# Kernel optimization log

Measured on AMD Instinct MI355X. Metric: run time of the kernel, lower is better.

## Reference

```python
import jax, jax.numpy as jnp
import numpy as np

H = 4096        # hidden_size
NH = 32         # heads
HD = H // NH    # head_dim = 128
EPS = 1e-5
MINUS_INF = -10000.0
B, S = 2, 1024


def setup_inputs() -> dict:
    key = jax.random.key(0)
    ks = jax.random.split(key, 7)
    x = jax.random.normal(ks[0], (B, S, H), jnp.float32)
    mask = jnp.zeros((B, 1, 1, S), jnp.float32)  # additive padding mask (0 = keep)
    norm_w = 1.0 + 0.02 * jax.random.normal(ks[1], (H,), jnp.float32)
    norm_b = 0.02 * jax.random.normal(ks[2], (H,), jnp.float32)
    qkv_w = 0.02 * jax.random.normal(ks[3], (H, 3 * H), jnp.float32)
    qkv_b = 0.02 * jax.random.normal(ks[4], (3 * H,), jnp.float32)
    attn_ow = 0.02 * jax.random.normal(ks[5], (H, H), jnp.float32)
    return {"x": x, "mask": mask, "norm_w": norm_w, "norm_b": norm_b,
            "qkv_w": qkv_w, "qkv_b": qkv_b, "attn_ow": attn_ow}


def reference(x, mask, norm_w, norm_b, qkv_w, qkv_b, attn_ow):
    b, s, h = x.shape
    # --- pre-attention layernorm (qkv_gemm fuses this in DeepSpeed) ---
    mu = jnp.mean(x, axis=-1, keepdims=True)
    var = jnp.mean(jnp.square(x - mu), axis=-1, keepdims=True)
    inp_norm = (x - mu) * jax.lax.rsqrt(var + EPS) * norm_w + norm_b
    # --- fused QKV GEMM + bias ---
    qkv = inp_norm @ qkv_w + qkv_b                      # [b, s, 3H]
    q, k, v = jnp.split(qkv, 3, axis=-1)
    q = q.reshape(b, s, NH, HD).transpose(0, 2, 1, 3)   # [b, nh, s, hd]
    k = k.reshape(b, s, NH, HD).transpose(0, 2, 1, 3)
    v = v.reshape(b, s, NH, HD).transpose(0, 2, 1, 3)
    # --- scaled dot-product with triangular (causal) mask + additive input mask ---
    norm_factor = 1.0 / jnp.sqrt(jnp.asarray(HD, x.dtype))
    scores = jnp.einsum('bhqd,bhkd->bhqk', q, k) * norm_factor  # [b, nh, s, s]
    causal = jnp.where(jnp.tril(jnp.ones((s, s), bool)), 0.0, MINUS_INF).astype(x.dtype)
    probs = jax.nn.softmax(scores + causal + mask, axis=-1)
    ctx = jnp.einsum('bhqk,bhkd->bhqd', probs, v)               # [b, nh, s, hd]
    ctx = ctx.transpose(0, 2, 1, 3).reshape(b, s, h)
    # --- output projection (vector_matmul, bias applied later in MLP residual-add) ---
    out = ctx @ attn_ow
    return out
```

## Files before the change

kernel.cpp:

```cpp
#include <hip/hip_runtime.h>
#include <stdint.h>


#define S_LEN 1024
#define HID   4096
#define NHEAD 32
#define HDIM  128

typedef __attribute__((ext_vector_type(8))) short bf16x8;
typedef __attribute__((ext_vector_type(4))) float f32x4;
typedef __attribute__((ext_vector_type(8))) unsigned short us8;

__device__ __forceinline__ unsigned short f2bf(float f) {
    union { float f; unsigned u; } v; v.f = f;
    unsigned r = v.u + 0x7fffu + ((v.u >> 16) & 1u);
    return (unsigned short)(r >> 16);
}

__device__ __forceinline__ void gld16(const unsigned short* g, unsigned short* l) {
    __builtin_amdgcn_global_load_lds(
        (const __attribute__((address_space(1))) void*)g,
        (__attribute__((address_space(3))) void*)l, 16, 0, 0);
}

__global__ __launch_bounds__(256) void ln_kernel(const float* __restrict__ x,
        const float* __restrict__ w, const float* __restrict__ bch,
        unsigned short* __restrict__ out) {
    const int row = blockIdx.x;
    const int t = threadIdx.x;
    const float* xr = x + (size_t)row * HID;
    float4 v[4];
    float sum = 0.f, sq = 0.f;
#pragma unroll
    for (int i = 0; i < 4; i++) {
        v[i] = ((const float4*)xr)[t + (i << 8)];
        sum += v[i].x + v[i].y + v[i].z + v[i].w;
        sq  += v[i].x*v[i].x + v[i].y*v[i].y + v[i].z*v[i].z + v[i].w*v[i].w;
    }
#pragma unroll
    for (int off = 32; off; off >>= 1) {
        sum += __shfl_down(sum, off);
        sq  += __shfl_down(sq, off);
    }
    __shared__ float ssum[4], ssq[4];
    if ((t & 63) == 0) { ssum[t >> 6] = sum; ssq[t >> 6] = sq; }
    __syncthreads();
    const float s_all = ssum[0] + ssum[1] + ssum[2] + ssum[3];
    const float q_all = ssq[0] + ssq[1] + ssq[2] + ssq[3];
    const float mean = s_all * (1.f / HID);
    const float var  = q_all * (1.f / HID) - mean * mean;
    const float rstd = rsqrtf(var + 1e-5f);
    unsigned short* orow = out + (size_t)row * HID;
#pragma unroll
    for (int i = 0; i < 4; i++) {
        float4 wv = ((const float4*)w)[t + (i << 8)];
        float4 bv = ((const float4*)bch)[t + (i << 8)];
        ushort4 o;
        o.x = f2bf((v[i].x - mean) * rstd * wv.x + bv.x);
        o.y = f2bf((v[i].y - mean) * rstd * wv.y + bv.y);
        o.z = f2bf((v[i].z - mean) * rstd * wv.z + bv.z);
        o.w = f2bf((v[i].w - mean) * rstd * wv.w + bv.w);
        ((ushort4*)orow)[t + (i << 8)] = o;
    }
}

__global__ __launch_bounds__(256) void transconv(const float* __restrict__ W,
        unsigned short* __restrict__ Wt, int K, int N) {
    __shared__ float tileT[128 * 65];
    const int n0 = blockIdx.x << 7, k0 = blockIdx.y << 6;
    const int t = threadIdx.x;
#pragma unroll
    for (int it = 0; it < 8; it++) {
        int idx = (it << 8) + t;
        int r = idx >> 5;
        int c4 = idx & 31;
        float4 v = *(const float4*)(W + (size_t)(k0 + r) * N + n0 + (c4 << 2));
        tileT[((c4 << 2) + 0) * 65 + r] = v.x;
        tileT[((c4 << 2) + 1) * 65 + r] = v.y;
        tileT[((c4 << 2) + 2) * 65 + r] = v.z;
        tileT[((c4 << 2) + 3) * 65 + r] = v.w;
    }
    __syncthreads();
#pragma unroll
    for (int it = 0; it < 4; it++) {
        int idx = (it << 8) + t;
        int n = idx >> 3;
        int k8 = idx & 7;
        const float* src = &tileT[n * 65 + (k8 << 3)];
        us8 o;
#pragma unroll
        for (int e = 0; e < 8; e++) o[e] = f2bf(src[e]);
        *(us8*)(Wt + (size_t)(n0 + n) * K + k0 + (k8 << 3)) = o;
    }
}


#define GEMM_PHASE(CB, KS, PFT, PFB, DO_VM)                                       \
  {                                                                               \
    bf16x8 af[4], bfv[4];                                                         \
    _Pragma("unroll") for (int ii = 0; ii < 4; ii++) af[ii] = ldA(CB, KS, ii);    \
    _Pragma("unroll") for (int jj = 0; jj < 4; jj++) bfv[jj] = ldB(CB, KS, jj);   \
    stageA(PFT, KS, PFB);                                                         \
    stageB(PFT, KS, PFB);                                                         \
    __builtin_amdgcn_s_barrier();                                                 \
    asm volatile("s_waitcnt lgkmcnt(0)" ::: "memory");                            \
    __builtin_amdgcn_sched_barrier(0);                                            \
    __builtin_amdgcn_s_setprio(1);                                                \
    _Pragma("unroll") for (int ii = 0; ii < 4; ii++)                              \
      _Pragma("unroll") for (int jj = 0; jj < 4; jj++)                            \
        acc[ii][jj] = __builtin_amdgcn_mfma_f32_16x16x32_bf16(                    \
            af[ii], bfv[jj], acc[ii][jj], 0, 0, 0);                               \
    __builtin_amdgcn_s_setprio(0);                                                \
    if (DO_VM) asm volatile("s_waitcnt vmcnt(6)" ::: "memory");                   \
    __builtin_amdgcn_s_barrier();                                                 \
  }

#define GEMM_TILE(TT, CB)                                                         \
  {                                                                               \
    int pf_ = (TT) + 2; if (pf_ > 63) pf_ = 63;                                   \
    GEMM_PHASE(CB, 0, pf_, ((CB) + 2) % 3, 0)                                     \
    GEMM_PHASE(CB, 1, pf_, ((CB) + 2) % 3, 1)                                     \
  }

__device__ __forceinline__ void gemm_core_8w(
        const unsigned short* __restrict__ GA,
        const unsigned short* __restrict__ GB,
        unsigned short* lds,
        f32x4 acc[4][4]) {
    const int t = threadIdx.x;
    const int wave = t >> 6, lane = t & 63, quad = lane >> 4, l16 = lane & 15;
    const int waveM = wave >> 2, waveN = wave & 3;
    const int srow = lane >> 2;
    const int scol = (((lane & 3) ^ ((lane >> 3) & 3)) << 3);

    auto stageA = [&](int tau, int ks, int buf) {
        const int row = (wave << 4) + srow;
        gld16(GA + ((size_t)row << 12) + (tau << 6) + (ks << 5) + scol,
              lds + buf * 24576 + (ks << 12) + (wave << 9));
    };
    auto stageB = [&](int tau, int ks, int buf) {
#pragma unroll
        for (int u = 0; u < 2; u++) {
            const int ii = (wave << 1) + u;
            const int row = (ii << 4) + srow;
            gld16(GB + ((size_t)row << 12) + (tau << 6) + (ks << 5) + scol,
                  lds + buf * 24576 + 8192 + (ks << 13) + (ii << 9));
        }
    };
    auto ldA = [&](int buf, int ks, int ii) -> bf16x8 {
        const int r = (waveM << 6) + (ii << 4) + l16;
        return ((const bf16x8*)(lds + buf * 24576 + (ks << 12)))
            [(r << 2) + (quad ^ ((r >> 1) & 3))];
    };
    auto ldB = [&](int buf, int ks, int jj) -> bf16x8 {
        const int r = (waveN << 6) + (jj << 4) + l16;
        return ((const bf16x8*)(lds + buf * 24576 + 8192 + (ks << 13)))
            [(r << 2) + (quad ^ ((r >> 1) & 3))];
    };

    stageA(0, 0, 0); stageB(0, 0, 0); stageA(0, 1, 0); stageB(0, 1, 0);
    stageA(1, 0, 1); stageB(1, 0, 1); stageA(1, 1, 1); stageB(1, 1, 1);
    asm volatile("s_waitcnt vmcnt(6)" ::: "memory");
    __builtin_amdgcn_s_barrier();

    for (int tb = 0; tb < 63; tb += 3) {
        GEMM_TILE(tb,     0)
        GEMM_TILE(tb + 1, 1)
        GEMM_TILE(tb + 2, 2)
    }
    GEMM_TILE(63, 0)
    asm volatile("s_waitcnt vmcnt(0)" ::: "memory");
}

__global__ __launch_bounds__(512, 2) void gemm_qkv8(
        const unsigned short* __restrict__ A,
        const unsigned short* __restrict__ Bt,
        const float* __restrict__ bias,
        unsigned short* __restrict__ qb,
        unsigned short* __restrict__ kb,
        unsigned short* __restrict__ vt) {
    __shared__ unsigned short lds[73728];
    const int orig = blockIdx.x;
    const int wg = ((orig & 7) * 96) + (orig >> 3);
    const int bm = wg / 48, bn = wg - bm * 48;
    const int t = threadIdx.x;
    const int wave = t >> 6, lane = t & 63, quad = lane >> 4, l16 = lane & 15;
    const int waveM = wave >> 2, waveN = wave & 3;

    const f32x4 fz = {0.f, 0.f, 0.f, 0.f};
    f32x4 acc[4][4];
#pragma unroll
    for (int i = 0; i < 4; i++)
#pragma unroll
        for (int j = 0; j < 4; j++) acc[i][j] = fz;

    gemm_core_8w(A + ((size_t)bm << 19), Bt + ((size_t)bn << 20), lds, acc);

    const int nbase = (bn << 8) + (waveN << 6);
    const int which = nbase >> 12;
#pragma unroll
    for (int ii = 0; ii < 4; ii++) {
#pragma unroll
        for (int jj = 0; jj < 4; jj++) {
#pragma unroll
            for (int r = 0; r < 4; r++) {
                int m = (bm << 7) + (waveM << 6) + (ii << 4) + (quad << 2) + r;
                int n = nbase + (jj << 4) + l16;
                float v = acc[ii][jj][r] + bias[n];
                unsigned short bvv = f2bf(v);
                int bb = m >> 10, s = m & 1023;
                int h = n & 4095, head = h >> 7, hd = h & 127;
                size_t bh = (size_t)(bb << 5) + head;
                if (which == 0)      qb[(bh * S_LEN + s) * HDIM + hd] = bvv;
                else if (which == 1) kb[(bh * S_LEN + s) * HDIM + hd] = bvv;
                else                 vt[(bh * HDIM + hd) * S_LEN + s] = bvv;
            }
        }
    }
}

__global__ __launch_bounds__(512, 2) void gemm_proj8(
        const unsigned short* __restrict__ A,
        const unsigned short* __restrict__ Bt,
        float* __restrict__ outf) {
    __shared__ unsigned short lds[73728];
    const int orig = blockIdx.x;
    const int wg = ((orig & 7) * 32) + (orig >> 3);
    const int bm = wg >> 4, bn = wg & 15;
    const int t = threadIdx.x;
    const int wave = t >> 6, lane = t & 63, quad = lane >> 4, l16 = lane & 15;
    const int waveM = wave >> 2, waveN = wave & 3;

    const f32x4 fz = {0.f, 0.f, 0.f, 0.f};
    f32x4 acc[4][4];
#pragma unroll
    for (int i = 0; i < 4; i++)
#pragma unroll
        for (int j = 0; j < 4; j++) acc[i][j] = fz;

    gemm_core_8w(A + ((size_t)bm << 19), Bt + ((size_t)bn << 20), lds, acc);

#pragma unroll
    for (int ii = 0; ii < 4; ii++)
#pragma unroll
        for (int jj = 0; jj < 4; jj++)
#pragma unroll
            for (int r = 0; r < 4; r++) {
                int m = (bm << 7) + (waveM << 6) + (ii << 4) + (quad << 2) + r;
                int n = (bn << 8) + (waveN << 6) + (jj << 4) + l16;
                outf[((size_t)m << 12) + n] = acc[ii][jj][r];
            }
}

__global__ __launch_bounds__(256) void attn_kernel(
        const unsigned short* __restrict__ qbuf,
        const unsigned short* __restrict__ kbuf,
        const unsigned short* __restrict__ vtbuf,
        const float* __restrict__ mask,
        unsigned short* __restrict__ ctx) {
    __shared__ unsigned short q_lds[64 * 128];
    __shared__ unsigned short k_lds[64 * 128];
    __shared__ unsigned short v_lds[128 * 64];
    __shared__ unsigned short p_lds[64 * 64];
    const int t = threadIdx.x;
    const int wave = t >> 6, lane = t & 63, quad = lane >> 4, l16 = lane & 15;
    const int bq = blockIdx.x, bh = blockIdx.y;
    const int q0 = bq << 6;
    const int b = bh >> 5;
    const unsigned short* Q  = qbuf  + (size_t)bh * S_LEN * HDIM;
    const unsigned short* Kp = kbuf  + (size_t)bh * S_LEN * HDIM;
    const unsigned short* Vp = vtbuf + (size_t)bh * HDIM * S_LEN;

    {
        int r = t >> 4, c = (t & 15) << 3;
#pragma unroll
        for (int it = 0; it < 4; it++)
            gld16(Q + (size_t)(q0 + r + (it << 4)) * HDIM + c,
                  q_lds + ((((it << 8) + (wave << 6))) << 3));
    }

    const f32x4 fz = {0.f, 0.f, 0.f, 0.f};
    f32x4 o[8];
#pragma unroll
    for (int n = 0; n < 8; n++) o[n] = fz;
    float l_i[4] = {0.f, 0.f, 0.f, 0.f};
    const float scale = 0.08838834764831845f;
    const float* mrow = mask + b * S_LEN;

    for (int kt = 0; kt <= bq; kt++) {
        const int k0 = kt << 6;
        {
            int rk = t >> 4, ck = (t & 15) << 3;
            int rv = t >> 3, cv = (t & 7) << 3;
#pragma unroll
            for (int it = 0; it < 4; it++) {
                gld16(Kp + (size_t)(k0 + rk + (it << 4)) * HDIM + ck,
                      k_lds + (((it << 8) + (wave << 6)) << 3));
                gld16(Vp + (size_t)(rv + (it << 5)) * S_LEN + k0 + cv,
                      v_lds + (((it << 8) + (wave << 6)) << 3));
            }
        }
        __syncthreads();

        f32x4 sacc[4];
#pragma unroll
        for (int j = 0; j < 4; j++) sacc[j] = fz;
        const bf16x8* qv = (const bf16x8*)q_lds;
        const bf16x8* kv = (const bf16x8*)k_lds;
#pragma unroll
        for (int kk = 0; kk < 4; kk++) {
            bf16x8 aq = qv[(((wave << 4) + l16) << 4) + (kk << 2) + quad];
#pragma unroll
            for (int j = 0; j < 4; j++) {
                bf16x8 bk = kv[((((j << 4) + l16)) << 4) + (kk << 2) + quad];
                sacc[j] = __builtin_amdgcn_mfma_f32_16x16x32_bf16(aq, bk, sacc[j], 0, 0, 0);
            }
        }

#pragma unroll
        for (int r = 0; r < 4; r++) {
            int qrow = q0 + (wave << 4) + (quad << 2) + r;
#pragma unroll
            for (int j = 0; j < 4; j++) {
                int key = k0 + (j << 4) + l16;
                float x = sacc[j][r] * scale + mrow[key];
                if (key > qrow) x -= 10000.0f;
                float p = __expf(x);
                l_i[r] += p;
                p_lds[((wave << 4) + (quad << 2) + r) * 64 + (j << 4) + l16] = f2bf(p);
            }
        }
        __syncthreads();

        const bf16x8* pvv = (const bf16x8*)p_lds;
        const bf16x8* vv = (const bf16x8*)v_lds;
#pragma unroll
        for (int ks = 0; ks < 2; ks++) {
            bf16x8 ap = pvv[(((wave << 4) + l16) << 3) + (ks << 2) + quad];
#pragma unroll
            for (int n = 0; n < 8; n++) {
                bf16x8 bvv = vv[((((n << 4) + l16)) << 3) + (ks << 2) + quad];
                o[n] = __builtin_amdgcn_mfma_f32_16x16x32_bf16(ap, bvv, o[n], 0, 0, 0);
            }
        }
        __syncthreads();
    }

#pragma unroll
    for (int r = 0; r < 4; r++) {
        float l = l_i[r];
#pragma unroll
        for (int off = 1; off < 16; off <<= 1) l += __shfl_xor(l, off);
        float inv = 1.0f / l;
        int qrow = q0 + (wave << 4) + (quad << 2) + r;
        size_t base = ((size_t)(b * S_LEN + qrow)) * HID + ((size_t)(bh & 31) << 7);
#pragma unroll
        for (int n = 0; n < 8; n++)
            ctx[base + (n << 4) + l16] = f2bf(o[n][r] * inv);
    }
}

extern "C" void kernel_launch(void* const* d_in, const int* in_sizes, int n_in,
                              void* d_out, int out_size, void* d_ws, size_t ws_size,
                              hipStream_t stream) {
    const float* x       = (const float*)d_in[0];
    const float* mask    = (const float*)d_in[1];
    const float* norm_w  = (const float*)d_in[2];
    const float* norm_b  = (const float*)d_in[3];
    const float* qkv_w   = (const float*)d_in[4];
    const float* qkv_b   = (const float*)d_in[5];
    const float* attn_ow = (const float*)d_in[6];
    float* out = (float*)d_out;

    char* ws = (char*)d_ws;
    size_t off = 0;
    auto alloc = [&](size_t bytes) {
        char* p = ws + off;
        off += (bytes + 255) & ~(size_t)255;
        return p;
    };
    unsigned short* inp_norm = (unsigned short*)alloc((size_t)2048 * HID * 2);
    unsigned short* qkv_wt   = (unsigned short*)alloc((size_t)3 * HID * HID * 2);
    unsigned short* ow_t     = (unsigned short*)alloc((size_t)HID * HID * 2);
    unsigned short* qb       = (unsigned short*)alloc((size_t)64 * S_LEN * HDIM * 2);
    unsigned short* kb       = (unsigned short*)alloc((size_t)64 * S_LEN * HDIM * 2);
    unsigned short* vt       = (unsigned short*)alloc((size_t)64 * S_LEN * HDIM * 2);
    unsigned short* ctx      = (unsigned short*)alloc((size_t)2048 * HID * 2);

    ln_kernel<<<2048, 256, 0, stream>>>(x, norm_w, norm_b, inp_norm);
    transconv<<<dim3(3 * HID / 128, HID / 64), 256, 0, stream>>>(qkv_w, qkv_wt, HID, 3 * HID);
    transconv<<<dim3(HID / 128, HID / 64), 256, 0, stream>>>(attn_ow, ow_t, HID, HID);
    gemm_qkv8<<<768, 512, 0, stream>>>(inp_norm, qkv_wt, qkv_b, qb, kb, vt);
    attn_kernel<<<dim3(16, 64), 256, 0, stream>>>(qb, kb, vt, mask, ctx);
    gemm_proj8<<<256, 512, 0, stream>>>(ctx, ow_t, out);
}
```

Before: 839.0 us.

## Enlarge QKV GEMM tile to 256x256 with new double-buffered core

Replaces the 128x256-tile QKV GEMM with a 256x256-tile version using a new double-buffered mainloop, where each wave computes 8x4 MFMA fragments and reuses its B fragments across two A halves. The grid drops from 768 to 384 workgroups, which halves redundant B-matrix loads and raises arithmetic intensity per LDS byte. In exchange it doubles the accumulator registers per wave, which may limit occupancy or cause spills, and 384 blocks may fill the CUs less evenly. Block ordering also changes to a simple bm-fastest mapping.

```diff
diff --git a/kernel.cpp b/kernel.cpp
--- a/kernel.cpp
+++ b/kernel.cpp
@@ -91,6 +91,127 @@
 #pragma unroll
         for (int e = 0; e < 8; e++) o[e] = f2bf(src[e]);
         *(us8*)(Wt + (size_t)(n0 + n) * K + k0 + (k8 << 3)) = o;
+    }
+}
+
+
+#define T256_PHASE(CB, KS, IH, READ_B, STAGE_CALL, DO_VM)                         \
+  {                                                                               \
+    _Pragma("unroll") for (int ii = 0; ii < 4; ii++)                              \
+        af[ii] = ldA(CB, KS, ((IH) << 2) + ii);                                   \
+    if (READ_B) {                                                                 \
+      _Pragma("unroll") for (int jj = 0; jj < 4; jj++) bfv[jj] = ldB(CB, KS, jj); \
+    }                                                                             \
+    STAGE_CALL;                                                                   \
+    __builtin_amdgcn_s_barrier();                                                 \
+    asm volatile("s_waitcnt lgkmcnt(0)" ::: "memory");                            \
+    __builtin_amdgcn_sched_barrier(0);                                            \
+    __builtin_amdgcn_s_setprio(1);                                                \
+    _Pragma("unroll") for (int ii = 0; ii < 4; ii++)                              \
+      _Pragma("unroll") for (int jj = 0; jj < 4; jj++)                            \
+        acc[((IH) << 2) + ii][jj] = __builtin_amdgcn_mfma_f32_16x16x32_bf16(      \
+            af[ii], bfv[jj], acc[((IH) << 2) + ii][jj], 0, 0, 0);                 \
+    __builtin_amdgcn_s_setprio(0);                                                \
+    if (DO_VM) asm volatile("s_waitcnt vmcnt(4)" ::: "memory");                   \
+    __builtin_amdgcn_s_barrier();                                                 \
+  }
+
+#define T256_TILE(TT, CB, PT)                                                     \
+  {                                                                               \
+    bf16x8 af[4], bfv[4];                                                         \
+    T256_PHASE(CB, 0, 0, 1, stage(GA, (((CB)^1) << 15)        , (PT), 0), 0)      \
+    T256_PHASE(CB, 0, 1, 0, stage(GB, (((CB)^1) << 15) + 16384, (PT), 0), 1)      \
+    T256_PHASE(CB, 1, 0, 1, stage(GA, (((CB)^1) << 15) +  8192, (PT), 1), 0)      \
+    T256_PHASE(CB, 1, 1, 0, stage(GB, (((CB)^1) << 15) + 24576, (PT), 1), 1)      \
+  }
+
+__device__ __forceinline__ void gemm_core_256(
+        const unsigned short* __restrict__ GA,
+        const unsigned short* __restrict__ GB,
+        unsigned short* lds,
+        f32x4 acc[8][4]) {
+    const int t = threadIdx.x;
+    const int wave = t >> 6, lane = t & 63, quad = lane >> 4, l16 = lane & 15;
+    const int waveM = wave >> 2, waveN = wave & 3;
+    const int sq8 = (((lane & 3) ^ ((lane >> 3) & 3)) << 3);
+
+    auto stage = [&](const unsigned short* G, int ldsOff, int tau, int ks) {
+#pragma unroll
+        for (int u = 0; u < 2; u++) {
+            const int grp = (u << 3) + wave;
+            const int r = (grp << 4) + (lane >> 2);
+            gld16(G + ((size_t)r << 12) + (tau << 6) + (ks << 5) + sq8,
+                  lds + ldsOff + (grp << 9));
+        }
+    };
+    auto ldA = [&](int buf, int ks, int i) -> bf16x8 {
+        const int r = (waveM << 7) + (i << 4) + l16;
+        return ((const bf16x8*)(lds + (buf << 15) + (ks << 13)))
+            [(r << 2) + (quad ^ ((r >> 1) & 3))];
+    };
+    auto ldB = [&](int buf, int ks, int j) -> bf16x8 {
+        const int r = (waveN << 6) + (j << 4) + l16;
+        return ((const bf16x8*)(lds + (buf << 15) + 16384 + (ks << 13)))
+            [(r << 2) + (quad ^ ((r >> 1) & 3))];
+    };
+
+    stage(GA, 0,     0, 0);
+    stage(GB, 16384, 0, 0);
+    stage(GA, 8192,  0, 1);
+    stage(GB, 24576, 0, 1);
+    asm volatile("s_waitcnt vmcnt(4)" ::: "memory");
+    __builtin_amdgcn_s_barrier();
+
+    for (int tt = 0; tt < 64; tt += 2) {
+        T256_TILE(tt,     0, tt + 1)
+        T256_TILE(tt + 1, 1, (tt == 62) ? 63 : tt + 2)
+    }
+    asm volatile("s_waitcnt vmcnt(0)" ::: "memory");
+}
+
+__global__ __launch_bounds__(512, 2) void gemm_qkv16(
+        const unsigned short* __restrict__ A,
+        const unsigned short* __restrict__ Bt,
+        const float* __restrict__ bias,
+        unsigned short* __restrict__ qb,
+        unsigned short* __restrict__ kb,
+        unsigned short* __restrict__ vt) {
+    __shared__ unsigned short lds[65536];
+    const int orig = blockIdx.x;
+    const int bm = orig & 7, bn = orig >> 3;
+    const int t = threadIdx.x;
+    const int wave = t >> 6, lane = t & 63, quad = lane >> 4, l16 = lane & 15;
+    const int waveM = wave >> 2, waveN = wave & 3;
+
+    const f32x4 fz = {0.f, 0.f, 0.f, 0.f};
+    f32x4 acc[8][4];
+#pragma unroll
+    for (int i = 0; i < 8; i++)
+#pragma unroll
+        for (int j = 0; j < 4; j++) acc[i][j] = fz;
+
+    gemm_core_256(A + ((size_t)bm << 20), Bt + ((size_t)bn << 20), lds, acc);
+
+    const int nbase = (bn << 8) + (waveN << 6);
+    const int which = nbase >> 12;
+#pragma unroll
+    for (int ii = 0; ii < 8; ii++) {
+#pragma unroll
+        for (int jj = 0; jj < 4; jj++) {
+#pragma unroll
+            for (int r = 0; r < 4; r++) {
+                int m = (bm << 8) + (waveM << 7) + (ii << 4) + (quad << 2) + r;
+                int n = nbase + (jj << 4) + l16;
+                float v = acc[ii][jj][r] + bias[n];
+                unsigned short bvv = f2bf(v);
+                int bb = m >> 10, s = m & 1023;
+                int h = n & 4095, head = h >> 7, hd = h & 127;
+                size_t bh = (size_t)(bb << 5) + head;
+                if (which == 0)      qb[(bh * S_LEN + s) * HDIM + hd] = bvv;
+                else if (which == 1) kb[(bh * S_LEN + s) * HDIM + hd] = bvv;
+                else                 vt[(bh * HDIM + hd) * S_LEN + s] = bvv;
+            }
+        }
     }
 }
 
@@ -172,53 +293,6 @@
     asm volatile("s_waitcnt vmcnt(0)" ::: "memory");
 }
 
-__global__ __launch_bounds__(512, 2) void gemm_qkv8(
-        const unsigned short* __restrict__ A,
-        const unsigned short* __restrict__ Bt,
-        const float* __restrict__ bias,
-        unsigned short* __restrict__ qb,
-        unsigned short* __restrict__ kb,
-        unsigned short* __restrict__ vt) {
-    __shared__ unsigned short lds[73728];
-    const int orig = blockIdx.x;
-    const int wg = ((orig & 7) * 96) + (orig >> 3);
-    const int bm = wg / 48, bn = wg - bm * 48;
-    const int t = threadIdx.x;
-    const int wave = t >> 6, lane = t & 63, quad = lane >> 4, l16 = lane & 15;
-    const int waveM = wave >> 2, waveN = wave & 3;
-
-    const f32x4 fz = {0.f, 0.f, 0.f, 0.f};
-    f32x4 acc[4][4];
-#pragma unroll
-    for (int i = 0; i < 4; i++)
-#pragma unroll
-        for (int j = 0; j < 4; j++) acc[i][j] = fz;
-
-    gemm_core_8w(A + ((size_t)bm << 19), Bt + ((size_t)bn << 20), lds, acc);
-
-    const int nbase = (bn << 8) + (waveN << 6);
-    const int which = nbase >> 12;
-#pragma unroll
-    for (int ii = 0; ii < 4; ii++) {
-#pragma unroll
-        for (int jj = 0; jj < 4; jj++) {
-#pragma unroll
-            for (int r = 0; r < 4; r++) {
-                int m = (bm << 7) + (waveM << 6) + (ii << 4) + (quad << 2) + r;
-                int n = nbase + (jj << 4) + l16;
-                float v = acc[ii][jj][r] + bias[n];
-                unsigned short bvv = f2bf(v);
-                int bb = m >> 10, s = m & 1023;
-                int h = n & 4095, head = h >> 7, hd = h & 127;
-                size_t bh = (size_t)(bb << 5) + head;
-                if (which == 0)      qb[(bh * S_LEN + s) * HDIM + hd] = bvv;
-                else if (which == 1) kb[(bh * S_LEN + s) * HDIM + hd] = bvv;
-                else                 vt[(bh * HDIM + hd) * S_LEN + s] = bvv;
-            }
-        }
-    }
-}
-
 __global__ __launch_bounds__(512, 2) void gemm_proj8(
         const unsigned short* __restrict__ A,
         const unsigned short* __restrict__ Bt,
@@ -390,7 +464,7 @@
     ln_kernel<<<2048, 256, 0, stream>>>(x, norm_w, norm_b, inp_norm);
     transconv<<<dim3(3 * HID / 128, HID / 64), 256, 0, stream>>>(qkv_w, qkv_wt, HID, 3 * HID);
     transconv<<<dim3(HID / 128, HID / 64), 256, 0, stream>>>(attn_ow, ow_t, HID, HID);
-    gemm_qkv8<<<768, 512, 0, stream>>>(inp_norm, qkv_wt, qkv_b, qb, kb, vt);
+    gemm_qkv16<<<384, 512, 0, stream>>>(inp_norm, qkv_wt, qkv_b, qb, kb, vt);
     attn_kernel<<<dim3(16, 64), 256, 0, stream>>>(qb, kb, vt, mask, ctx);
     gemm_proj8<<<256, 512, 0, stream>>>(ctx, ow_t, out);
 }
```

New measurement: 810.5 us. 1.04x faster.

## Retile QKV and projection GEMMs and XOR-swizzle attention LDS layouts

Applied to the files above, without the earlier changes.

The QKV GEMM moves from 128x256 tiles with K=64 steps to 256x192 tiles with K=32 steps and a triple-buffered prefetch. That gives 512 blocks instead of 768, more reuse per block, and a simpler block mapping. The projection GEMM moves to 256x128 tiles with single-phase K=32 steps and a smaller LDS footprint. The attention kernel adds XOR swizzling to its Q/K/V/P LDS layouts to reduce bank conflicts. The tradeoffs are higher register pressure from the 8x3 accumulators, uneven load counts across waves, and more barriers per unit of K work.

```diff
diff --git a/kernel.cpp b/kernel.cpp
--- a/kernel.cpp
+++ b/kernel.cpp
@@ -95,141 +95,179 @@
 }
 
 
-#define GEMM_PHASE(CB, KS, PFT, PFB, DO_VM)                                       \
+#define QK_TILE(TT, CURB, PFB)                                                    \
   {                                                                               \
-    bf16x8 af[4], bfv[4];                                                         \
-    _Pragma("unroll") for (int ii = 0; ii < 4; ii++) af[ii] = ldA(CB, KS, ii);    \
-    _Pragma("unroll") for (int jj = 0; jj < 4; jj++) bfv[jj] = ldB(CB, KS, jj);   \
-    stageA(PFT, KS, PFB);                                                         \
-    stageB(PFT, KS, PFB);                                                         \
+    int pf_ = (TT) + 2; if (pf_ > 127) pf_ = 127;                                 \
+    stgA(pf_, PFB); stgB(pf_, PFB);                                               \
+    bf16x8 bfv[3], af[8];                                                         \
+    _Pragma("unroll") for (int jj = 0; jj < 3; jj++) bfv[jj] = ldB(CURB, jj);     \
+    _Pragma("unroll") for (int ii = 0; ii < 8; ii++) af[ii] = ldA(CURB, ii);      \
+    __builtin_amdgcn_s_setprio(1);                                                \
+    _Pragma("unroll") for (int ii = 0; ii < 8; ii++)                              \
+      _Pragma("unroll") for (int jj = 0; jj < 3; jj++)                            \
+        acc[ii][jj] = __builtin_amdgcn_mfma_f32_16x16x32_bf16(                    \
+            af[ii], bfv[jj], acc[ii][jj], 0, 0, 0);                               \
+    __builtin_amdgcn_s_setprio(0);                                                \
+    if (wave < 4) { asm volatile("s_waitcnt vmcnt(4)" ::: "memory"); }            \
+    else          { asm volatile("s_waitcnt vmcnt(3)" ::: "memory"); }            \
     __builtin_amdgcn_s_barrier();                                                 \
-    asm volatile("s_waitcnt lgkmcnt(0)" ::: "memory");                            \
-    __builtin_amdgcn_sched_barrier(0);                                            \
+  }
+
+__global__ __launch_bounds__(512, 2) void gemm_qkv32(
+        const unsigned short* __restrict__ A,
+        const unsigned short* __restrict__ Bt,
+        const float* __restrict__ bias,
+        unsigned short* __restrict__ qb,
+        unsigned short* __restrict__ kb,
+        unsigned short* __restrict__ vt) {
+    __shared__ unsigned short lds[43008];
+    const int orig = blockIdx.x;
+    const int bm = orig & 7, bn = orig >> 3;
+    const int t = threadIdx.x;
+    const int wave = t >> 6, lane = t & 63, quad = lane >> 4, l16 = lane & 15;
+    const int waveM = wave >> 2, waveN = wave & 3;
+
+    const unsigned short* GA = A  + ((size_t)bm << 8) * HID;
+    const unsigned short* GB = Bt + ((size_t)bn * 192) * HID;
+
+    const int swz  = (((lane & 3) ^ ((lane >> 3) & 3)) << 3);
+    const int arow = lane >> 2;
+
+    auto stgA = [&](int tt, int buf) {
+#pragma unroll
+        for (int u = 0; u < 2; u++) {
+            const int g = (wave << 1) + u;
+            gld16(GA + (size_t)((g << 4) + arow) * HID + (tt << 5) + swz,
+                  lds + buf * 14336 + (g << 9));
+        }
+    };
+    auto stgB = [&](int tt, int buf) {
+        if (wave < 4) {
+#pragma unroll
+            for (int u = 0; u < 2; u++) {
+                const int g = (wave << 1) + u;
+                gld16(GB + (size_t)((g << 4) + arow) * HID + (tt << 5) + swz,
+                      lds + buf * 14336 + 8192 + (g << 9));
+            }
+        } else {
+            const int g = wave + 4;
+            gld16(GB + (size_t)((g << 4) + arow) * HID + (tt << 5) + swz,
+                  lds + buf * 14336 + 8192 + (g << 9));
+        }
+    };
+    auto ldA = [&](int buf, int i) -> bf16x8 {
+        const int r = (waveM << 7) + (i << 4) + l16;
+        return ((const bf16x8*)lds)
+            [((buf * 14336) >> 3) + (r << 2) + (quad ^ ((r >> 1) & 3))];
+    };
+    auto ldB = [&](int buf, int j) -> bf16x8 {
+        const int r = waveN * 48 + (j << 4) + l16;
+        return ((const bf16x8*)lds)
+            [((buf * 14336 + 8192) >> 3) + (r << 2) + (quad ^ ((r >> 1) & 3))];
+    };
+
+    const f32x4 fz = {0.f, 0.f, 0.f, 0.f};
+    f32x4 acc[8][3];
+#pragma unroll
+    for (int i = 0; i < 8; i++)
+#pragma unroll
+        for (int j = 0; j < 3; j++) acc[i][j] = fz;
+
+    stgA(0, 0); stgB(0, 0);
+    stgA(1, 1); stgB(1, 1);
+    if (wave < 4) { asm volatile("s_waitcnt vmcnt(4)" ::: "memory"); }
+    else          { asm volatile("s_waitcnt vmcnt(3)" ::: "memory"); }
+    __builtin_amdgcn_s_barrier();
+
+    for (int tt = 0; tt < 126; tt += 3) {
+        QK_TILE(tt,     0, 2)
+        QK_TILE(tt + 1, 1, 0)
+        QK_TILE(tt + 2, 2, 1)
+    }
+    QK_TILE(126, 0, 2)
+    QK_TILE(127, 1, 0)
+    asm volatile("s_waitcnt vmcnt(0)" ::: "memory");
+
+#pragma unroll
+    for (int ii = 0; ii < 8; ii++) {
+#pragma unroll
+        for (int jj = 0; jj < 3; jj++) {
+#pragma unroll
+            for (int r = 0; r < 4; r++) {
+                int m = (bm << 8) + (waveM << 7) + (ii << 4) + (quad << 2) + r;
+                int n = bn * 192 + waveN * 48 + (jj << 4) + l16;
+                float v = acc[ii][jj][r] + bias[n];
+                unsigned short bvv = f2bf(v);
+                int bb = m >> 10, s = m & 1023;
+                int which = n >> 12;
+                int h = n & 4095, head = h >> 7, hd = h & 127;
+                size_t bh = (size_t)(bb << 5) + head;
+                if (which == 0)      qb[(bh * S_LEN + s) * HDIM + hd] = bvv;
+                else if (which == 1) kb[(bh * S_LEN + s) * HDIM + hd] = bvv;
+                else                 vt[(bh * HDIM + hd) * S_LEN + s] = bvv;
+            }
+        }
+    }
+}
+
+
+#define PJ_TILE(TT, CURB, PFB)                                                    \
+  {                                                                               \
+    int pf_ = (TT) + 2; if (pf_ > 127) pf_ = 127;                                 \
+    stgA(pf_, PFB); stgB(pf_, PFB);                                               \
+    bf16x8 bfv[4], af[4];                                                         \
+    _Pragma("unroll") for (int jj = 0; jj < 4; jj++) bfv[jj] = ldB(CURB, jj);     \
+    _Pragma("unroll") for (int ii = 0; ii < 4; ii++) af[ii] = ldA(CURB, ii);      \
     __builtin_amdgcn_s_setprio(1);                                                \
     _Pragma("unroll") for (int ii = 0; ii < 4; ii++)                              \
       _Pragma("unroll") for (int jj = 0; jj < 4; jj++)                            \
         acc[ii][jj] = __builtin_amdgcn_mfma_f32_16x16x32_bf16(                    \
             af[ii], bfv[jj], acc[ii][jj], 0, 0, 0);                               \
     __builtin_amdgcn_s_setprio(0);                                                \
-    if (DO_VM) asm volatile("s_waitcnt vmcnt(6)" ::: "memory");                   \
+    asm volatile("s_waitcnt vmcnt(3)" ::: "memory");                              \
     __builtin_amdgcn_s_barrier();                                                 \
   }
 
-#define GEMM_TILE(TT, CB)                                                         \
-  {                                                                               \
-    int pf_ = (TT) + 2; if (pf_ > 63) pf_ = 63;                                   \
-    GEMM_PHASE(CB, 0, pf_, ((CB) + 2) % 3, 0)                                     \
-    GEMM_PHASE(CB, 1, pf_, ((CB) + 2) % 3, 1)                                     \
-  }
-
-__device__ __forceinline__ void gemm_core_8w(
-        const unsigned short* __restrict__ GA,
-        const unsigned short* __restrict__ GB,
-        unsigned short* lds,
-        f32x4 acc[4][4]) {
-    const int t = threadIdx.x;
-    const int wave = t >> 6, lane = t & 63, quad = lane >> 4, l16 = lane & 15;
-    const int waveM = wave >> 2, waveN = wave & 3;
-    const int srow = lane >> 2;
-    const int scol = (((lane & 3) ^ ((lane >> 3) & 3)) << 3);
-
-    auto stageA = [&](int tau, int ks, int buf) {
-        const int row = (wave << 4) + srow;
-        gld16(GA + ((size_t)row << 12) + (tau << 6) + (ks << 5) + scol,
-              lds + buf * 24576 + (ks << 12) + (wave << 9));
-    };
-    auto stageB = [&](int tau, int ks, int buf) {
-#pragma unroll
-        for (int u = 0; u < 2; u++) {
-            const int ii = (wave << 1) + u;
-            const int row = (ii << 4) + srow;
-            gld16(GB + ((size_t)row << 12) + (tau << 6) + (ks << 5) + scol,
-                  lds + buf * 24576 + 8192 + (ks << 13) + (ii << 9));
-        }
-    };
-    auto ldA = [&](int buf, int ks, int ii) -> bf16x8 {
-        const int r = (waveM << 6) + (ii << 4) + l16;
-        return ((const bf16x8*)(lds + buf * 24576 + (ks << 12)))
-            [(r << 2) + (quad ^ ((r >> 1) & 3))];
-    };
-    auto ldB = [&](int buf, int ks, int jj) -> bf16x8 {
-        const int r = (waveN << 6) + (jj << 4) + l16;
-        return ((const bf16x8*)(lds + buf * 24576 + 8192 + (ks << 13)))
-            [(r << 2) + (quad ^ ((r >> 1) & 3))];
-    };
-
-    stageA(0, 0, 0); stageB(0, 0, 0); stageA(0, 1, 0); stageB(0, 1, 0);
-    stageA(1, 0, 1); stageB(1, 0, 1); stageA(1, 1, 1); stageB(1, 1, 1);
-    asm volatile("s_waitcnt vmcnt(6)" ::: "memory");
-    __builtin_amdgcn_s_barrier();
-
-    for (int tb = 0; tb < 63; tb += 3) {
-        GEMM_TILE(tb,     0)
-        GEMM_TILE(tb + 1, 1)
-        GEMM_TILE(tb + 2, 2)
-    }
-    GEMM_TILE(63, 0)
-    asm volatile("s_waitcnt vmcnt(0)" ::: "memory");
-}
-
-__global__ __launch_bounds__(512, 2) void gemm_qkv8(
-        const unsigned short* __restrict__ A,
-        const unsigned short* __restrict__ Bt,
-        const float* __restrict__ bias,
-        unsigned short* __restrict__ qb,
-        unsigned short* __restrict__ kb,
-        unsigned short* __restrict__ vt) {
-    __shared__ unsigned short lds[73728];
-    const int orig = blockIdx.x;
-    const int wg = ((orig & 7) * 96) + (orig >> 3);
-    const int bm = wg / 48, bn = wg - bm * 48;
-    const int t = threadIdx.x;
-    const int wave = t >> 6, lane = t & 63, quad = lane >> 4, l16 = lane & 15;
-    const int waveM = wave >> 2, waveN = wave & 3;
-
-    const f32x4 fz = {0.f, 0.f, 0.f, 0.f};
-    f32x4 acc[4][4];
-#pragma unroll
-    for (int i = 0; i < 4; i++)
-#pragma unroll
-        for (int j = 0; j < 4; j++) acc[i][j] = fz;
-
-    gemm_core_8w(A + ((size_t)bm << 19), Bt + ((size_t)bn << 20), lds, acc);
-
-    const int nbase = (bn << 8) + (waveN << 6);
-    const int which = nbase >> 12;
-#pragma unroll
-    for (int ii = 0; ii < 4; ii++) {
-#pragma unroll
-        for (int jj = 0; jj < 4; jj++) {
-#pragma unroll
-            for (int r = 0; r < 4; r++) {
-                int m = (bm << 7) + (waveM << 6) + (ii << 4) + (quad << 2) + r;
-                int n = nbase + (jj << 4) + l16;
-                float v = acc[ii][jj][r] + bias[n];
-                unsigned short bvv = f2bf(v);
-                int bb = m >> 10, s = m & 1023;
-                int h = n & 4095, head = h >> 7, hd = h & 127;
-                size_t bh = (size_t)(bb << 5) + head;
-                if (which == 0)      qb[(bh * S_LEN + s) * HDIM + hd] = bvv;
-                else if (which == 1) kb[(bh * S_LEN + s) * HDIM + hd] = bvv;
-                else                 vt[(bh * HDIM + hd) * S_LEN + s] = bvv;
-            }
-        }
-    }
-}
-
-__global__ __launch_bounds__(512, 2) void gemm_proj8(
+__global__ __launch_bounds__(512, 2) void gemm_proj32(
         const unsigned short* __restrict__ A,
         const unsigned short* __restrict__ Bt,
         float* __restrict__ outf) {
-    __shared__ unsigned short lds[73728];
+    __shared__ unsigned short lds[36864];
     const int orig = blockIdx.x;
-    const int wg = ((orig & 7) * 32) + (orig >> 3);
-    const int bm = wg >> 4, bn = wg & 15;
+    const int bm = orig & 7, bn = orig >> 3;
     const int t = threadIdx.x;
     const int wave = t >> 6, lane = t & 63, quad = lane >> 4, l16 = lane & 15;
-    const int waveM = wave >> 2, waveN = wave & 3;
+    const int waveM = wave >> 1, waveN = wave & 1;
+
+    const unsigned short* GA = A  + ((size_t)bm << 8) * HID;
+    const unsigned short* GB = Bt + ((size_t)bn << 7) * HID;
+
+    const int swz  = (((lane & 3) ^ ((lane >> 3) & 3)) << 3);
+    const int arow = lane >> 2;
+
+    auto stgA = [&](int tt, int buf) {
+#pragma unroll
+        for (int u = 0; u < 2; u++) {
+            const int g = (wave << 1) + u;
+            gld16(GA + (size_t)((g << 4) + arow) * HID + (tt << 5) + swz,
+                  lds + buf * 12288 + (g << 9));
+        }
+    };
+    auto stgB = [&](int tt, int buf) {
+        const int g = wave;
+        gld16(GB + (size_t)((g << 4) + arow) * HID + (tt << 5) + swz,
+              lds + buf * 12288 + 8192 + (g << 9));
+    };
+    auto ldA = [&](int buf, int i) -> bf16x8 {
+        const int r = (waveM << 6) + (i << 4) + l16;
+        return ((const bf16x8*)lds)
+            [((buf * 12288) >> 3) + (r << 2) + (quad ^ ((r >> 1) & 3))];
+    };
+    auto ldB = [&](int buf, int j) -> bf16x8 {
+        const int r = (waveN << 6) + (j << 4) + l16;
+        return ((const bf16x8*)lds)
+            [((buf * 12288 + 8192) >> 3) + (r << 2) + (quad ^ ((r >> 1) & 3))];
+    };
 
     const f32x4 fz = {0.f, 0.f, 0.f, 0.f};
     f32x4 acc[4][4];
@@ -238,7 +276,19 @@
 #pragma unroll
         for (int j = 0; j < 4; j++) acc[i][j] = fz;
 
-    gemm_core_8w(A + ((size_t)bm << 19), Bt + ((size_t)bn << 20), lds, acc);
+    stgA(0, 0); stgB(0, 0);
+    stgA(1, 1); stgB(1, 1);
+    asm volatile("s_waitcnt vmcnt(3)" ::: "memory");
+    __builtin_amdgcn_s_barrier();
+
+    for (int tt = 0; tt < 126; tt += 3) {
+        PJ_TILE(tt,     0, 2)
+        PJ_TILE(tt + 1, 1, 0)
+        PJ_TILE(tt + 2, 2, 1)
+    }
+    PJ_TILE(126, 0, 2)
+    PJ_TILE(127, 1, 0)
+    asm volatile("s_waitcnt vmcnt(0)" ::: "memory");
 
 #pragma unroll
     for (int ii = 0; ii < 4; ii++)
@@ -246,8 +296,8 @@
         for (int jj = 0; jj < 4; jj++)
 #pragma unroll
             for (int r = 0; r < 4; r++) {
-                int m = (bm << 7) + (waveM << 6) + (ii << 4) + (quad << 2) + r;
-                int n = (bn << 8) + (waveN << 6) + (jj << 4) + l16;
+                int m = (bm << 8) + (waveM << 6) + (ii << 4) + (quad << 2) + r;
+                int n = (bn << 7) + (waveN << 6) + (jj << 4) + l16;
                 outf[((size_t)m << 12) + n] = acc[ii][jj][r];
             }
 }
@@ -272,7 +322,8 @@
     const unsigned short* Vp = vtbuf + (size_t)bh * HDIM * S_LEN;
 
     {
-        int r = t >> 4, c = (t & 15) << 3;
+        int r = t >> 4;
+        int c = (((t & 15) ^ ((t >> 4) & 7)) << 3);
 #pragma unroll
         for (int it = 0; it < 4; it++)
             gld16(Q + (size_t)(q0 + r + (it << 4)) * HDIM + c,
@@ -290,8 +341,8 @@
     for (int kt = 0; kt <= bq; kt++) {
         const int k0 = kt << 6;
         {
-            int rk = t >> 4, ck = (t & 15) << 3;
-            int rv = t >> 3, cv = (t & 7) << 3;
+            int rk = t >> 4, ck = (((t & 15) ^ ((t >> 4) & 7)) << 3);
+            int rv = t >> 3, cv = (((t & 7) ^ ((t >> 3) & 7)) << 3);
 #pragma unroll
             for (int it = 0; it < 4; it++) {
                 gld16(Kp + (size_t)(k0 + rk + (it << 4)) * HDIM + ck,
@@ -309,17 +360,18 @@
         const bf16x8* kv = (const bf16x8*)k_lds;
 #pragma unroll
         for (int kk = 0; kk < 4; kk++) {
-            bf16x8 aq = qv[(((wave << 4) + l16) << 4) + (kk << 2) + quad];
+            bf16x8 aq = qv[(((wave << 4) + l16) << 4) + (((kk << 2) + quad) ^ (l16 & 7))];
 #pragma unroll
             for (int j = 0; j < 4; j++) {
-                bf16x8 bk = kv[((((j << 4) + l16)) << 4) + (kk << 2) + quad];
+                bf16x8 bk = kv[((((j << 4) + l16)) << 4) + (((kk << 2) + quad) ^ (l16 & 7))];
                 sacc[j] = __builtin_amdgcn_mfma_f32_16x16x32_bf16(aq, bk, sacc[j], 0, 0, 0);
             }
         }
 
 #pragma unroll
         for (int r = 0; r < 4; r++) {
-            int qrow = q0 + (wave << 4) + (quad << 2) + r;
+            int prow = (wave << 4) + (quad << 2) + r;
+            int qrow = q0 + prow;
 #pragma unroll
             for (int j = 0; j < 4; j++) {
                 int key = k0 + (j << 4) + l16;
@@ -327,7 +379,8 @@
                 if (key > qrow) x -= 10000.0f;
                 float p = __expf(x);
                 l_i[r] += p;
-                p_lds[((wave << 4) + (quad << 2) + r) * 64 + (j << 4) + l16] = f2bf(p);
+                int pc = (j << 1) + (l16 >> 3);
+                p_lds[(prow << 6) + ((pc ^ (prow & 7)) << 3) + (l16 & 7)] = f2bf(p);
             }
         }
         __syncthreads();
@@ -336,10 +389,10 @@
         const bf16x8* vv = (const bf16x8*)v_lds;
 #pragma unroll
         for (int ks = 0; ks < 2; ks++) {
-            bf16x8 ap = pvv[(((wave << 4) + l16) << 3) + (ks << 2) + quad];
+            bf16x8 ap = pvv[(((wave << 4) + l16) << 3) + (((ks << 2) + quad) ^ (l16 & 7))];
 #pragma unroll
             for (int n = 0; n < 8; n++) {
-                bf16x8 bvv = vv[((((n << 4) + l16)) << 3) + (ks << 2) + quad];
+                bf16x8 bvv = vv[((((n << 4) + l16)) << 3) + (((ks << 2) + quad) ^ (l16 & 7))];
                 o[n] = __builtin_amdgcn_mfma_f32_16x16x32_bf16(ap, bvv, o[n], 0, 0, 0);
             }
         }
@@ -390,7 +443,7 @@
     ln_kernel<<<2048, 256, 0, stream>>>(x, norm_w, norm_b, inp_norm);
     transconv<<<dim3(3 * HID / 128, HID / 64), 256, 0, stream>>>(qkv_w, qkv_wt, HID, 3 * HID);
     transconv<<<dim3(HID / 128, HID / 64), 256, 0, stream>>>(attn_ow, ow_t, HID, HID);
-    gemm_qkv8<<<768, 512, 0, stream>>>(inp_norm, qkv_wt, qkv_b, qb, kb, vt);
+    gemm_qkv32<<<512, 512, 0, stream>>>(inp_norm, qkv_wt, qkv_b, qb, kb, vt);
     attn_kernel<<<dim3(16, 64), 256, 0, stream>>>(qb, kb, vt, mask, ctx);
-    gemm_proj8<<<256, 512, 0, stream>>>(ctx, ow_t, out);
-}
+    gemm_proj32<<<256, 512, 0, stream>>>(ctx, ow_t, out);
+}
```

Measured after the change: 715.4 us. 14.7% less time.
